# Kernel tuning notes

Hardware: AMD Instinct MI355X
Metric: run time of the kernel (lower is better)

Reference implementation:

```python
import jax, jax.numpy as jnp
import numpy as np

SEQ_LEN = 600
N_CLASSES = 5
P = 6  # max_ar_order


def setup_inputs() -> dict:
    key = jax.random.key(0)
    N = 32768
    x = jax.random.normal(key, (N, SEQ_LEN), dtype=jnp.float32)
    return {"x": x}


def reference(x):
    N = x.shape[0]
    T_out = SEQ_LEN - P
    # Lag matrix: X_lag[:, t, k] = x[:, P-1-k + t]  -> [N, T_out, P]
    X_lag = jnp.stack([x[:, P - 1 - k:SEQ_LEN - 1 - k] for k in range(P)], axis=-1)
    y = x[:, P:]  # [N, T_out]
    ones = jnp.ones((N, T_out, 1), dtype=x.dtype)
    D = jnp.concatenate([ones, X_lag], axis=-1)  # [N, T_out, P+1]
    # Least squares via normal equations (tiny (P+1)x(P+1) batched solve)
    G = jnp.einsum('ntk,ntl->nkl', D, D)        # [N, P+1, P+1]
    b = jnp.einsum('ntk,nt->nk', D, y)          # [N, P+1]
    w = jnp.linalg.solve(G, b[..., None])[..., 0]  # [N, P+1]
    y_hat_valid = jnp.einsum('ntk,nk->nt', D, w)   # [N, T_out]
    x_hat = jnp.zeros((N, SEQ_LEN), dtype=x.dtype).at[:, P:].set(y_hat_valid)
    ar_coeffs = w[:, 1:]  # [N, P]
    coeffs = jnp.broadcast_to(ar_coeffs[:, None, :], (N, SEQ_LEN, P))
    # zero the first P time steps
    t_mask = (jnp.arange(SEQ_LEN) >= P).astype(x.dtype)[None, :, None]
    coeffs = coeffs * t_mask
    p_logits = jnp.zeros((N, N_CLASSES), dtype=x.dtype)
    p_hard = jnp.zeros((N,), dtype=jnp.int32)
    return (coeffs, p_logits, p_hard, x_hat)
```

## Files before the change

### kernel.cpp

```cpp
#include <hip/hip_runtime.h>

#define SEQ 600
#define PP 6
#define TOUT 594
#define NF4 150
#define NF4P 152

typedef float v4f __attribute__((ext_vector_type(4)));

__device__ __forceinline__ void nt_store4(float4* p, float4 v) {
    v4f vv;
    vv.x = v.x; vv.y = v.y; vv.z = v.z; vv.w = v.w;
    __builtin_nontemporal_store(vv, reinterpret_cast<v4f*>(p));
}

__global__ __launch_bounds__(256) void ar_all_kernel(
    const float* __restrict__ x,
    float* __restrict__ coeffs,
    float* __restrict__ extra,
    float* __restrict__ x_hat,
    int N)
{
    __shared__ __align__(16) float4 sxr[4][NF4P];

    const int wave = threadIdx.x >> 6;
    const int lane = threadIdx.x & 63;
    const int row  = (blockIdx.x << 2) + wave;

    float4* s4 = sxr[wave];

    {
        const float4* xr = reinterpret_cast<const float4*>(x + (size_t)row * SEQ);
        float4 r0, r1, r2;
        int m0 = lane, m1 = lane + 64, m2 = lane + 128;
        r0 = xr[m0];
        r1 = xr[m1];
        if (m2 < NF4) r2 = xr[m2];
        s4[m0] = r0;
        s4[m1] = r1;
        if (m2 < NF4) s4[m2] = r2;
        if (lane < 2) s4[NF4 + lane] = make_float4(0.f, 0.f, 0.f, 0.f);
    }
    __syncthreads();

    float S = 0.f;
    float Q[7] = {0.f, 0.f, 0.f, 0.f, 0.f, 0.f, 0.f};
    #pragma unroll
    for (int k = 0; k < 3; ++k) {
        const int m = lane + 64 * k;
        if (m < NF4) {
            float4 a = s4[m], b = s4[m + 1], c = s4[m + 2];
            float W[12] = {a.x, a.y, a.z, a.w, b.x, b.y, b.z, b.w,
                           c.x, c.y, c.z, c.w};
            #pragma unroll
            for (int cc = 0; cc < 4; ++cc) {
                S += W[cc];
                #pragma unroll
                for (int d = 0; d < 7; ++d) Q[d] += W[cc] * W[cc + d];
            }
        }
    }
    #pragma unroll
    for (int m = 1; m < 64; m <<= 1) {
        S += __shfl_xor(S, m, 64);
        #pragma unroll
        for (int d = 0; d < 7; ++d) Q[d] += __shfl_xor(Q[d], m, 64);
    }

    float low[8], hig[16];
    {
        float4 e0 = s4[0], e1 = s4[1];
        float4 t0 = s4[148], t1 = s4[149], t2 = s4[150], t3 = s4[151];
        low[0]=e0.x; low[1]=e0.y; low[2]=e0.z; low[3]=e0.w;
        low[4]=e1.x; low[5]=e1.y; low[6]=e1.z; low[7]=e1.w;
        hig[0]=t0.x; hig[1]=t0.y; hig[2]=t0.z; hig[3]=t0.w;
        hig[4]=t1.x; hig[5]=t1.y; hig[6]=t1.z; hig[7]=t1.w;
        hig[8]=t2.x; hig[9]=t2.y; hig[10]=t2.z; hig[11]=t2.w;
        hig[12]=t3.x; hig[13]=t3.y; hig[14]=t3.z; hig[15]=t3.w;
    }
    float pre[8], suf[8];
    pre[0] = 0.f; suf[0] = 0.f;
    #pragma unroll
    for (int c = 1; c < 8; ++c) {
        pre[c] = pre[c - 1] + low[c - 1];
        suf[c] = suf[c - 1] + hig[8 - c];
    }

    float M[7][7];
    float rhs[7];
    M[0][0] = (float)TOUT;
    #pragma unroll
    for (int k = 0; k < 6; ++k) {
        float v = S - pre[5 - k] - suf[k + 1];
        M[k + 1][0] = v; M[0][k + 1] = v;
    }
    #pragma unroll
    for (int k = 0; k < 6; ++k) {
        #pragma unroll
        for (int l = k; l < 6; ++l) {
            const int a = 5 - l, d = l - k;
            float head = 0.f;
            #pragma unroll
            for (int i = 0; i < a; ++i) head += low[i] * low[i + d];
            float tail = 0.f;
            #pragma unroll
            for (int i = a + TOUT; i < SEQ; ++i)
                tail += hig[i - 592] * hig[i + d - 592];
            float v = Q[d] - head - tail;
            M[l + 1][k + 1] = v; M[k + 1][l + 1] = v;
        }
    }
    rhs[0] = S - pre[6];
    #pragma unroll
    for (int k = 0; k < 6; ++k) {
        const int a = 5 - k, d = k + 1;
        float head = 0.f;
        #pragma unroll
        for (int i = 0; i < a; ++i) head += low[i] * low[i + d];
        float tail = 0.f;
        #pragma unroll
        for (int i = a + TOUT; i < SEQ; ++i)
            tail += hig[i - 592] * hig[i + d - 592];
        rhs[k + 1] = Q[d] - head - tail;
    }

    float invd[7];
    #pragma unroll
    for (int j = 0; j < 7; ++j) {
        float s = M[j][j];
        #pragma unroll
        for (int m = 0; m < j; ++m) s -= M[j][m] * M[j][m];
        float ljj = sqrtf(s);
        M[j][j] = ljj;
        float inv = __builtin_amdgcn_rcpf(ljj);
        invd[j] = inv;
        #pragma unroll
        for (int i2 = j + 1; i2 < 7; ++i2) {
            float s2 = M[i2][j];
            #pragma unroll
            for (int m = 0; m < j; ++m) s2 -= M[i2][m] * M[j][m];
            M[i2][j] = s2 * inv;
        }
    }
    float w[7], z[7];
    #pragma unroll
    for (int i2 = 0; i2 < 7; ++i2) {
        float s = rhs[i2];
        #pragma unroll
        for (int m = 0; m < i2; ++m) s -= M[i2][m] * z[m];
        z[i2] = s * invd[i2];
    }
    #pragma unroll
    for (int i2 = 6; i2 >= 0; --i2) {
        float s = z[i2];
        #pragma unroll
        for (int m = i2 + 1; m < 7; ++m) s -= M[m][i2] * w[m];
        w[i2] = s * invd[i2];
    }

    if (lane < 5) extra[(size_t)5 * row + lane] = 0.f;
    if (lane == 5) extra[(size_t)5 * N + row] = 0.f;

    {
        const float4 P0 = make_float4(w[1], w[2], w[3], w[4]);
        const float4 P1 = make_float4(w[5], w[6], w[1], w[2]);
        const float4 P2 = make_float4(w[3], w[4], w[5], w[6]);
        const int r0 = lane % 3;
        const float4 A0 = (r0 == 0) ? P0 : ((r0 == 1) ? P1 : P2);
        const float4 A1 = (r0 == 0) ? P1 : ((r0 == 1) ? P2 : P0);
        const float4 A2 = (r0 == 0) ? P2 : ((r0 == 1) ? P0 : P1);

        float4* crow = reinterpret_cast<float4*>(coeffs + (size_t)row * (SEQ * PP));
        float4 v0 = (lane <= 8) ? make_float4(0.f, 0.f, 0.f, 0.f) : A0;
        nt_store4(crow + lane, v0);
        #pragma unroll
        for (int j = 1; j < 14; ++j) {
            const float4 v = (j % 3 == 0) ? A0 : ((j % 3 == 1) ? A1 : A2);
            nt_store4(crow + lane + 64 * j, v);
        }
        if (lane < 4) nt_store4(crow + lane + 64 * 14, A2);
    }

    {
        float4* xh4 = reinterpret_cast<float4*>(x_hat + (size_t)row * SEQ);
        #pragma unroll
        for (int k = 0; k < 3; ++k) {
            const int m = lane + 64 * k;
            if (m < NF4) {
                float4 v;
                if (m == 0) {
                    v = make_float4(0.f, 0.f, 0.f, 0.f);
                } else {
                    const int mm2 = (m >= 2) ? (m - 2) : 0;
                    float4 ra = s4[mm2], rb = s4[m - 1], rc = s4[m];
                    float W[12] = {ra.x, ra.y, ra.z, ra.w, rb.x, rb.y, rb.z, rb.w,
                                   rc.x, rc.y, rc.z, rc.w};
                    float p[4];
                    #pragma unroll
                    for (int c = 0; c < 4; ++c) {
                        float s = w[0];
                        #pragma unroll
                        for (int kk = 1; kk <= 6; ++kk) s += w[kk] * W[8 + c - kk];
                        p[c] = s;
                    }
                    if (m == 1) { p[0] = 0.f; p[1] = 0.f; }
                    v = make_float4(p[0], p[1], p[2], p[3]);
                }
                nt_store4(xh4 + m, v);
            }
        }
    }
}

extern "C" void kernel_launch(void* const* d_in, const int* in_sizes, int n_in,
                              void* d_out, int out_size, void* d_ws, size_t ws_size,
                              hipStream_t stream) {
    const float* x = (const float*)d_in[0];
    const int N = in_sizes[0] / SEQ;

    float* out    = (float*)d_out;
    float* coeffs = out;
    float* extra  = out + (size_t)N * SEQ * PP;
    float* x_hat  = extra + (size_t)N * 6;

    ar_all_kernel<<<dim3(N / 4), dim3(256), 0, stream>>>(x, coeffs, extra, x_hat, N);
}
```

Baseline: 598.7 us.

## Use DPP wave reductions, nontemporal loads, regular stores, and trim tail reads

```diff
diff --git a/kernel.cpp b/kernel.cpp
--- a/kernel.cpp
+++ b/kernel.cpp
@@ -8,10 +8,19 @@
 
 typedef float v4f __attribute__((ext_vector_type(4)));
 
-__device__ __forceinline__ void nt_store4(float4* p, float4 v) {
-    v4f vv;
-    vv.x = v.x; vv.y = v.y; vv.z = v.z; vv.w = v.w;
-    __builtin_nontemporal_store(vv, reinterpret_cast<v4f*>(p));
+template<int CTRL>
+__device__ __forceinline__ float dpp_mov(float v) {
+    return __int_as_float(__builtin_amdgcn_update_dpp(
+        0, __float_as_int(v), CTRL, 0xF, 0xF, true));
+}
+__device__ __forceinline__ float wave_sum(float v) {
+    v += dpp_mov<0x111>(v);
+    v += dpp_mov<0x112>(v);
+    v += dpp_mov<0x114>(v);
+    v += dpp_mov<0x118>(v);
+    v += dpp_mov<0x142>(v);
+    v += dpp_mov<0x143>(v);
+    return __int_as_float(__builtin_amdgcn_readlane(__float_as_int(v), 63));
 }
 
 __global__ __launch_bounds__(256) void ar_all_kernel(
@@ -21,25 +30,25 @@
     float* __restrict__ x_hat,
     int N)
 {
-    __shared__ __align__(16) float4 sxr[4][NF4P];
+    __shared__ __align__(16) v4f sxr[4][NF4P];
 
     const int wave = threadIdx.x >> 6;
     const int lane = threadIdx.x & 63;
     const int row  = (blockIdx.x << 2) + wave;
 
-    float4* s4 = sxr[wave];
-
-    {
-        const float4* xr = reinterpret_cast<const float4*>(x + (size_t)row * SEQ);
-        float4 r0, r1, r2;
-        int m0 = lane, m1 = lane + 64, m2 = lane + 128;
-        r0 = xr[m0];
-        r1 = xr[m1];
-        if (m2 < NF4) r2 = xr[m2];
-        s4[m0] = r0;
-        s4[m1] = r1;
+    v4f* s4 = sxr[wave];
+
+    {
+        const v4f* xr = reinterpret_cast<const v4f*>(x + (size_t)row * SEQ);
+        v4f r0 = __builtin_nontemporal_load(xr + lane);
+        v4f r1 = __builtin_nontemporal_load(xr + lane + 64);
+        v4f r2;
+        const int m2 = lane + 128;
+        if (m2 < NF4) r2 = __builtin_nontemporal_load(xr + m2);
+        s4[lane] = r0;
+        s4[lane + 64] = r1;
         if (m2 < NF4) s4[m2] = r2;
-        if (lane < 2) s4[NF4 + lane] = make_float4(0.f, 0.f, 0.f, 0.f);
+        if (lane < 2) { v4f z = {0.f, 0.f, 0.f, 0.f}; s4[NF4 + lane] = z; }
     }
     __syncthreads();
 
@@ -49,7 +58,7 @@
     for (int k = 0; k < 3; ++k) {
         const int m = lane + 64 * k;
         if (m < NF4) {
-            float4 a = s4[m], b = s4[m + 1], c = s4[m + 2];
+            v4f a = s4[m], b = s4[m + 1], c = s4[m + 2];
             float W[12] = {a.x, a.y, a.z, a.w, b.x, b.y, b.z, b.w,
                            c.x, c.y, c.z, c.w};
             #pragma unroll
@@ -60,23 +69,18 @@
             }
         }
     }
-    #pragma unroll
-    for (int m = 1; m < 64; m <<= 1) {
-        S += __shfl_xor(S, m, 64);
-        #pragma unroll
-        for (int d = 0; d < 7; ++d) Q[d] += __shfl_xor(Q[d], m, 64);
-    }
-
-    float low[8], hig[16];
-    {
-        float4 e0 = s4[0], e1 = s4[1];
-        float4 t0 = s4[148], t1 = s4[149], t2 = s4[150], t3 = s4[151];
+    S = wave_sum(S);
+    #pragma unroll
+    for (int d = 0; d < 7; ++d) Q[d] = wave_sum(Q[d]);
+
+    float low[8], hig[8];
+    {
+        v4f e0 = s4[0], e1 = s4[1];
+        v4f t0 = s4[148], t1 = s4[149];
         low[0]=e0.x; low[1]=e0.y; low[2]=e0.z; low[3]=e0.w;
         low[4]=e1.x; low[5]=e1.y; low[6]=e1.z; low[7]=e1.w;
         hig[0]=t0.x; hig[1]=t0.y; hig[2]=t0.z; hig[3]=t0.w;
         hig[4]=t1.x; hig[5]=t1.y; hig[6]=t1.z; hig[7]=t1.w;
-        hig[8]=t2.x; hig[9]=t2.y; hig[10]=t2.z; hig[11]=t2.w;
-        hig[12]=t3.x; hig[13]=t3.y; hig[14]=t3.z; hig[15]=t3.w;
     }
     float pre[8], suf[8];
     pre[0] = 0.f; suf[0] = 0.f;
@@ -105,7 +109,7 @@
             float tail = 0.f;
             #pragma unroll
             for (int i = a + TOUT; i < SEQ; ++i)
-                tail += hig[i - 592] * hig[i + d - 592];
+                if (i + d < SEQ) tail += hig[i - 592] * hig[i + d - 592];
             float v = Q[d] - head - tail;
             M[l + 1][k + 1] = v; M[k + 1][l + 1] = v;
         }
@@ -120,7 +124,7 @@
         float tail = 0.f;
         #pragma unroll
         for (int i = a + TOUT; i < SEQ; ++i)
-            tail += hig[i - 592] * hig[i + d - 592];
+            if (i + d < SEQ) tail += hig[i - 592] * hig[i + d - 592];
         rhs[k + 1] = Q[d] - head - tail;
     }
 
@@ -158,41 +162,38 @@
         w[i2] = s * invd[i2];
     }
 
-    if (lane < 5) extra[(size_t)5 * row + lane] = 0.f;
-    if (lane == 5) extra[(size_t)5 * N + row] = 0.f;
-
-    {
-        const float4 P0 = make_float4(w[1], w[2], w[3], w[4]);
-        const float4 P1 = make_float4(w[5], w[6], w[1], w[2]);
-        const float4 P2 = make_float4(w[3], w[4], w[5], w[6]);
+    {
+        const v4f P0 = {w[1], w[2], w[3], w[4]};
+        const v4f P1 = {w[5], w[6], w[1], w[2]};
+        const v4f P2 = {w[3], w[4], w[5], w[6]};
         const int r0 = lane % 3;
-        const float4 A0 = (r0 == 0) ? P0 : ((r0 == 1) ? P1 : P2);
-        const float4 A1 = (r0 == 0) ? P1 : ((r0 == 1) ? P2 : P0);
-        const float4 A2 = (r0 == 0) ? P2 : ((r0 == 1) ? P0 : P1);
-
-        float4* crow = reinterpret_cast<float4*>(coeffs + (size_t)row * (SEQ * PP));
-        float4 v0 = (lane <= 8) ? make_float4(0.f, 0.f, 0.f, 0.f) : A0;
-        nt_store4(crow + lane, v0);
+        const v4f A0 = (r0 == 0) ? P0 : ((r0 == 1) ? P1 : P2);
+        const v4f A1 = (r0 == 0) ? P1 : ((r0 == 1) ? P2 : P0);
+        const v4f A2 = (r0 == 0) ? P2 : ((r0 == 1) ? P0 : P1);
+
+        v4f* crow = reinterpret_cast<v4f*>(coeffs + (size_t)row * (SEQ * PP));
+        v4f zz = {0.f, 0.f, 0.f, 0.f};
+        crow[lane] = (lane <= 8) ? zz : A0;
         #pragma unroll
         for (int j = 1; j < 14; ++j) {
-            const float4 v = (j % 3 == 0) ? A0 : ((j % 3 == 1) ? A1 : A2);
-            nt_store4(crow + lane + 64 * j, v);
-        }
-        if (lane < 4) nt_store4(crow + lane + 64 * 14, A2);
-    }
-
-    {
-        float4* xh4 = reinterpret_cast<float4*>(x_hat + (size_t)row * SEQ);
+            crow[lane + 64 * j] = (j % 3 == 0) ? A0 : ((j % 3 == 1) ? A1 : A2);
+        }
+        if (lane < 4) crow[lane + 64 * 14] = A2;
+    }
+
+    {
+        v4f* xh4 = reinterpret_cast<v4f*>(x_hat + (size_t)row * SEQ);
         #pragma unroll
         for (int k = 0; k < 3; ++k) {
             const int m = lane + 64 * k;
             if (m < NF4) {
-                float4 v;
+                v4f v;
                 if (m == 0) {
-                    v = make_float4(0.f, 0.f, 0.f, 0.f);
+                    v4f zz = {0.f, 0.f, 0.f, 0.f};
+                    v = zz;
                 } else {
                     const int mm2 = (m >= 2) ? (m - 2) : 0;
-                    float4 ra = s4[mm2], rb = s4[m - 1], rc = s4[m];
+                    v4f ra = s4[mm2], rb = s4[m - 1], rc = s4[m];
                     float W[12] = {ra.x, ra.y, ra.z, ra.w, rb.x, rb.y, rb.z, rb.w,
                                    rc.x, rc.y, rc.z, rc.w};
                     float p[4];
@@ -204,12 +205,15 @@
                         p[c] = s;
                     }
                     if (m == 1) { p[0] = 0.f; p[1] = 0.f; }
-                    v = make_float4(p[0], p[1], p[2], p[3]);
+                    v.x = p[0]; v.y = p[1]; v.z = p[2]; v.w = p[3];
                 }
-                nt_store4(xh4 + m, v);
+                xh4[m] = v;
             }
         }
     }
+
+    if (lane < 5) extra[(size_t)5 * row + lane] = 0.f;
+    if (lane == 5) extra[(size_t)5 * N + row] = 0.f;
 }
 
 extern "C" void kernel_launch(void* const* d_in, const int* in_sizes, int n_in,
```

Result: no change. 593.3 us (-0.9%).
